# Kernel tuning notes

Hardware: AMD Instinct MI355X
Metric: run time of the kernel (lower is better)

The kernel has to match this reference:

```python
import jax, jax.numpy as jnp
import numpy as np

B, T, W, D = 4, 1000, 32, 200
ED, N, DCONV, DTR = 400, 16, 4, 13  # d_inner=2*d_model, d_state, d_conv, dt_rank=ceil(200/16)


def _causal_conv(x, w, b):
    # x: (B, L, ED), depthwise causal conv, kernel DCONV
    L = x.shape[1]
    xp = jnp.pad(x, ((0, 0), (DCONV - 1, 0), (0, 0)))
    y = sum(xp[:, k:k + L, :] * w[:, k] for k in range(DCONV))
    return y + b


def _ssm(x, A_log, Dp, xproj, dtw, dtb):
    # selective scan; x: (B, L, ED)
    A = -jnp.exp(A_log)                      # (ED, N)
    dbc = x @ xproj                          # (B, L, DTR+2N)
    delta, Bm, Cm = dbc[..., :DTR], dbc[..., DTR:DTR + N], dbc[..., DTR + N:]
    dt = jax.nn.softplus(delta @ dtw + dtb)  # (B, L, ED)
    dA = jnp.exp(dt[..., None] * A)                         # (B, L, ED, N)
    dBx = dt[..., None] * Bm[:, :, None, :] * x[..., None]  # (B, L, ED, N)

    def step(h, t):
        dA_t, dBx_t, C_t = t
        h = dA_t * h + dBx_t
        y = jnp.einsum('ben,bn->be', h, C_t)
        return h, y

    h0 = jnp.zeros((x.shape[0], ED, N), x.dtype)
    xs = (dA.transpose(1, 0, 2, 3), dBx.transpose(1, 0, 2, 3), Cm.transpose(1, 0, 2))
    _, ys = jax.lax.scan(step, h0, xs)
    return ys.transpose(1, 0, 2) + Dp * x


def _branch(x, in_proj, conv_w, conv_b, xproj, dtw, dtb, A_log, Dp):
    xz = x @ in_proj
    xp, z = xz[..., :ED], xz[..., ED:]
    xp = jax.nn.silu(_causal_conv(xp, conv_w, conv_b))
    y = _ssm(xp, A_log, Dp, xproj, dtw, dtb)
    return y * jax.nn.silu(z)


def setup_inputs() -> dict:
    key = jax.random.key(0)
    ks = jax.random.split(key, 24)
    s = 0.02
    nrm = lambda k, shape: jax.random.normal(k, shape, jnp.float32) * s
    inp = {}
    inp['input_ids'] = jax.random.normal(ks[0], (B, T, W, D), jnp.float32)
    inp['n_tweets'] = jax.random.randint(ks[1], (B,), 1, T + 1)
    inp['n_words'] = jax.random.randint(ks[2], (B, T), 1, W + 1)
    inp['cls_token'] = jnp.zeros((1, 1, D), jnp.float32)
    inp['w_attn'] = nrm(ks[3], (D, 1))
    inp['b_attn'] = jnp.zeros((1,), jnp.float32)
    inp['norm_w'] = jnp.ones((D,), jnp.float32)
    for i, d in enumerate(('f', 'b')):
        o = i * 8
        inp[f'in_proj_{d}'] = nrm(ks[4 + o], (D, 2 * ED))
        inp[f'conv_w_{d}'] = nrm(ks[5 + o], (ED, DCONV))
        inp[f'conv_b_{d}'] = jnp.zeros((ED,), jnp.float32)
        inp[f'xproj_{d}'] = nrm(ks[6 + o], (ED, DTR + 2 * N))
        inp[f'dtw_{d}'] = nrm(ks[7 + o], (DTR, ED))
        inp[f'dtb_{d}'] = jnp.zeros((ED,), jnp.float32)
        inp[f'A_log_{d}'] = jnp.log(jnp.broadcast_to(jnp.arange(1, N + 1, dtype=jnp.float32), (ED, N)))
        inp[f'D_{d}'] = jnp.ones((ED,), jnp.float32)
    inp['out_proj'] = nrm(ks[20], (ED, D))
    inp['head_w'] = nrm(ks[21], (D, 1))
    inp['head_b'] = jnp.zeros((1,), jnp.float32)
    return inp


def reference(input_ids, n_tweets, n_words, cls_token, w_attn, b_attn, norm_w,
              in_proj_f, conv_w_f, conv_b_f, xproj_f, dtw_f, dtb_f, A_log_f, D_f,
              in_proj_b, conv_w_b, conv_b_b, xproj_b, dtw_b, dtb_b, A_log_b, D_b,
              out_proj, head_w, head_b):
    Bz, Tz, Wz, Dz = input_ids.shape
    # ragged per-tweet attention pooling, fully vectorized with masks
    scores = jnp.squeeze(input_ids @ w_attn, -1) + b_attn[0]        # (B, T, W)
    wmask = jnp.arange(Wz) < n_words[..., None]                     # (B, T, W)
    scores = jnp.where(wmask, scores, -jnp.inf)
    attn = jax.nn.softmax(scores, axis=-1)
    tw = jnp.einsum('btw,btwd->btd', attn, input_ids)               # (B, T, D)
    tmask = jnp.arange(Tz) < n_tweets[:, None]
    tw = jnp.where(tmask[..., None], tw, 0.0)                       # padded tweets stay zero
    pos = Tz // 2
    x = jnp.concatenate([tw[:, :pos], jnp.broadcast_to(cls_token, (Bz, 1, Dz)), tw[:, pos:]], axis=1)
    # one bidirectional Mamba layer: pre-RMSNorm residual block
    xn = x * jax.lax.rsqrt(jnp.mean(x * x, axis=-1, keepdims=True) + 1e-5) * norm_w
    y_f = _branch(xn, in_proj_f, conv_w_f, conv_b_f, xproj_f, dtw_f, dtb_f, A_log_f, D_f)
    y_b = jnp.flip(_branch(jnp.flip(xn, 1), in_proj_b, conv_w_b, conv_b_b, xproj_b, dtw_b, dtb_b, A_log_b, D_b), 1)
    x = x + (y_f + y_b) @ out_proj
    logit = jnp.squeeze(x[:, pos] @ head_w, -1) + head_b[0]
    return jax.nn.sigmoid(logit)
```

## Files before the change

kernel.cpp:

```cpp
#include <hip/hip_runtime.h>
#include <cmath>

#define Bz 4
#define Tz 1000
#define Wz 32
#define Dz 200
#define EDz 400
#define Nz 16
#define DTRz 13
#define Lz 1001
#define POSz 500
#define LPz 501
#define TSTR 512
#define NEE 7
#define NEG_BIG -1e30f

__device__ __forceinline__ float wave_sum(float v) {
#pragma unroll
  for (int o = 32; o; o >>= 1) v += __shfl_xor(v, o);
  return v;
}

__global__ __launch_bounds__(256) void k_front(
    const float* __restrict__ x, const int* __restrict__ n_tweets,
    const int* __restrict__ n_words, const float* __restrict__ w_attn,
    const float* __restrict__ b_attn, const float* __restrict__ norm_w,
    const float* __restrict__ cls, const float* __restrict__ out_proj,
    const float* __restrict__ head_w, const float* __restrict__ ipf,
    const float* __restrict__ ipb, float* __restrict__ xn,
    float* __restrict__ zbuf, float* __restrict__ vbuf) {
  int bid = blockIdx.x;
  int tid = threadIdx.x;
  int wave = tid >> 6, lane = tid & 63;
  if (bid < 9) {
    if (bid == 0) {
      __shared__ float hw[Dz];
      if (tid < Dz) hw[tid] = head_w[tid];
      __syncthreads();
      for (int e = tid; e < EDz; e += 256) {
        float acc = 0.f;
        for (int d = 0; d < Dz; d += 4) {
          float4 ov = *(const float4*)(out_proj + e * Dz + d);
          acc += ov.x * hw[d] + ov.y * hw[d + 1] + ov.z * hw[d + 2] + ov.w * hw[d + 3];
        }
        vbuf[e] = acc;
      }
      return;
    }
    int id = bid - 1;
    int br = id >> 2, b = id & 3;
    __shared__ float xs[Dz];
    __shared__ float s_red[4];
    float val = (tid < Dz) ? cls[tid] : 0.f;
    float sq = wave_sum(val * val);
    if ((tid & 63) == 0) s_red[tid >> 6] = sq;
    __syncthreads();
    float tot = s_red[0] + s_red[1] + s_red[2] + s_red[3];
    float scale = rsqrtf(tot * (1.f / Dz) + 1e-5f);
    if (tid < Dz) {
      float o = val * scale * norm_w[tid];
      xs[tid] = o;
      if (br == 0) xn[((size_t)b * Lz + POSz) * Dz + tid] = o;
    }
    __syncthreads();
    const float* ip = br ? ipb : ipf;
    for (int e = tid; e < EDz; e += 256) {
      float acc = 0.f;
      for (int d = 0; d < Dz; ++d) acc += xs[d] * ip[d * (2 * EDz) + EDz + e];
      zbuf[((size_t)br * Bz + b) * EDz + e] = acc;
    }
    return;
  }
  int bt = (bid - 9) * 4 + wave;
  int b = bt / Tz, t = bt - b * Tz;
  int l = (t < POSz) ? t : t + 1;
  float* outr = xn + ((size_t)b * Lz + l) * Dz;
  int ntw = n_tweets[b]; if (ntw > Tz) ntw = Tz;
  if (t >= ntw) {
    if (lane < 50) *(float4*)(outr + lane * 4) = make_float4(0.f, 0.f, 0.f, 0.f);
    return;
  }
  int nw = n_words[b * Tz + t]; if (nw > Wz) nw = Wz; if (nw < 1) nw = 1;
  const float* xs = x + ((size_t)(b * Tz + t)) * (Wz * Dz);
  int h = lane & 1, w = lane >> 1;
  float sc = 0.f;
  if (w < nw) {
    const float* xr = xs + w * Dz + h * 100;
    const float* wr = w_attn + h * 100;
#pragma unroll
    for (int i = 0; i < 25; ++i) {
      float4 xv = *(const float4*)(xr + i * 4);
      float4 wv = *(const float4*)(wr + i * 4);
      sc += xv.x * wv.x + xv.y * wv.y + xv.z * wv.z + xv.w * wv.w;
    }
  }
  sc += __shfl_xor(sc, 1);
  float scv = (w < nw) ? (sc + b_attn[0]) : NEG_BIG;
  float m = scv;
#pragma unroll
  for (int o = 32; o; o >>= 1) m = fmaxf(m, __shfl_xor(m, o));
  float en = __expf(scv - m);
  float es = (h == 0) ? en : 0.f;
  float tot = wave_sum(es);
  en /= tot;
  float4 val = make_float4(0.f, 0.f, 0.f, 0.f);
  const float* xc = xs + lane * 4;
  for (int ww = 0; ww < nw; ++ww) {
    float aw = __shfl(en, 2 * ww);
    if (lane < 50) {
      float4 xv = *(const float4*)(xc + ww * Dz);
      val.x += aw * xv.x; val.y += aw * xv.y;
      val.z += aw * xv.z; val.w += aw * xv.w;
    }
  }
  float sq = (lane < 50) ? (val.x * val.x + val.y * val.y + val.z * val.z + val.w * val.w) : 0.f;
  sq = wave_sum(sq);
  float scale = rsqrtf(sq * (1.f / Dz) + 1e-5f);
  if (lane < 50) {
    float4 nw4 = *(const float4*)(norm_w + lane * 4);
    float4 o = make_float4(val.x * scale * nw4.x, val.y * scale * nw4.y,
                           val.z * scale * nw4.z, val.w * scale * nw4.w);
    *(float4*)(outr + lane * 4) = o;
  }
}

__global__ __launch_bounds__(256) void k_gemmid(
    const float* __restrict__ xn,
    const float* __restrict__ ipf, const float* __restrict__ ipb,
    const float* __restrict__ cwf, const float* __restrict__ cwb,
    const float* __restrict__ cbf, const float* __restrict__ cbb,
    const float* __restrict__ xpjf, const float* __restrict__ xpjb,
    float* __restrict__ xp_t, float* __restrict__ dbcp) {
  int bid = blockIdx.x;
  int ee = bid % NEE;
  int rem = bid / NEE;
  int tt = rem & 7, brb = rem >> 3;
  int br = brb >> 2, b = brb & 3;
  int t0 = tt * 64, e0 = ee * 64;
  int tid = threadIdx.x;
  int wave = tid >> 6, lane = tid & 63;
  const float* ip = br ? ipb : ipf;
  const float* cw = br ? cwb : cwf;
  const float* cb = br ? cbb : cbf;
  const float* xpj = br ? xpjb : xpjf;

  __shared__ float Xs[16][85];
  __shared__ float Ws[16][68];
  __shared__ float Pl[80][69];
  __shared__ float sred[4][64][45];

  int tx = tid & 15, ty = tid >> 4;
  float acc[5][4];
#pragma unroll
  for (int i = 0; i < 5; ++i)
#pragma unroll
    for (int j = 0; j < 4; ++j) acc[i][j] = 0.f;

  for (int dk = 0; dk < 200; dk += 16) {
    float xv[5];
#pragma unroll
    for (int r = 0; r < 5; ++r) {
      int trow = r * 16 + ty;
      int t = t0 - 8 + trow;
      int d = dk + tx;
      float v = 0.f;
      if (t >= 0 && t < LPz && d < Dz) {
        int l = br ? (Lz - 1 - t) : t;
        v = xn[((size_t)b * Lz + l) * Dz + d];
      }
      xv[r] = v;
    }
    int dw = dk + ty;
    int e4 = e0 + tx * 4;
    float wv[4];
#pragma unroll
    for (int c = 0; c < 4; ++c) {
      int e = e4 + c;
      wv[c] = (dw < Dz && e < EDz) ? ip[(size_t)dw * (2 * EDz) + e] : 0.f;
    }
    __syncthreads();
#pragma unroll
    for (int r = 0; r < 5; ++r) Xs[tx][r * 16 + ty] = xv[r];
#pragma unroll
    for (int c = 0; c < 4; ++c) Ws[ty][tx * 4 + c] = wv[c];
    __syncthreads();
#pragma unroll
    for (int k = 0; k < 16; ++k) {
      float av[5], bv[4];
#pragma unroll
      for (int i = 0; i < 5; ++i) av[i] = Xs[k][ty * 5 + i];
#pragma unroll
      for (int j = 0; j < 4; ++j) bv[j] = Ws[k][tx * 4 + j];
#pragma unroll
      for (int i = 0; i < 5; ++i)
#pragma unroll
        for (int j = 0; j < 4; ++j) acc[i][j] += av[i] * bv[j];
    }
  }
  __syncthreads();
#pragma unroll
  for (int i = 0; i < 5; ++i)
#pragma unroll
    for (int j = 0; j < 4; ++j) Pl[ty * 5 + i][tx * 4 + j] = acc[i][j];
  __syncthreads();

  float accq[45];
#pragma unroll
  for (int q = 0; q < 45; ++q) accq[q] = 0.f;
  int t = t0 + lane;
#pragma unroll 2
  for (int i = 0; i < 16; ++i) {
    int e_loc = wave * 16 + i;
    int e = e0 + e_loc;
    if (e < EDz) {
      int row = lane + 8;
      float p0 = Pl[row - 3][e_loc];
      float p1 = Pl[row - 2][e_loc];
      float p2 = Pl[row - 1][e_loc];
      float p3 = Pl[row][e_loc];
      float4 c4 = *(const float4*)(cw + e * 4);
      float a = cb[e] + c4.x * p0 + c4.y * p1 + c4.z * p2 + c4.w * p3;
      float sp = a / (1.f + __expf(-a));
      xp_t[((size_t)brb * EDz + e) * TSTR + t] = sp;
      const float* xq = xpj + e * 45;
#pragma unroll
      for (int q = 0; q < 45; ++q) accq[q] += sp * xq[q];
    }
  }
#pragma unroll
  for (int q = 0; q < 45; ++q) sred[wave][lane][q] = accq[q];
  __syncthreads();
  if (wave < 2) {
#pragma unroll
    for (int q = 0; q < 45; ++q)
      sred[wave][lane][q] += sred[wave + 2][lane][q];
  }
  __syncthreads();
  if (wave == 0) {
    float* dp = dbcp + ((size_t)(ee * 8 + brb) * 45) * TSTR + t;
#pragma unroll
    for (int q = 0; q < 45; ++q)
      dp[(size_t)q * TSTR] = sred[0][lane][q] + sred[1][lane][q];
  }
}

__global__ __launch_bounds__(256) void k_dt3(
    const float* __restrict__ dbcp, float* __restrict__ dfin_g,
    float* __restrict__ Bm_t, float* __restrict__ Cend) {
  int bid = blockIdx.x;
  int rg = bid & 3;
  int rem = bid >> 2;
  int tc = rem & 7, brb = rem >> 3;
  int tid = threadIdx.x;
  const size_t espstr = (size_t)8 * 45 * TSTR;
  int r0 = rg * 8;
  int nrows = (rg == 3) ? 5 : 8;
  for (int idx = tid; idx < nrows * 64; idx += 256) {
    int rl = idx >> 6, tl = idx & 63;
    int row = r0 + rl;
    size_t base = ((size_t)brb * 45 + row) * TSTR + tc * 64 + tl;
    float s = 0.f;
#pragma unroll
    for (int p = 0; p < NEE; ++p) s += dbcp[base + p * espstr];
    int tg = tc * 64 + tl;
    if (row < DTRz) dfin_g[((size_t)brb * DTRz + row) * TSTR + tg] = s;
    else Bm_t[((size_t)brb * Nz + (row - DTRz)) * TSTR + tg] = s;
  }
  if (rg == 3 && tc == 7 && tid < Nz) {
    size_t base = ((size_t)brb * 45 + 29 + tid) * TSTR + POSz;
    float s = 0.f;
#pragma unroll
    for (int p = 0; p < NEE; ++p) s += dbcp[base + p * espstr];
    Cend[brb * Nz + tid] = s;
  }
}

__global__ __launch_bounds__(64) void k_scan3(
    const float* __restrict__ xp_t, const float* __restrict__ dfin_g,
    const float* __restrict__ Bm_t, const float* __restrict__ Cend,
    const float* __restrict__ Alogf, const float* __restrict__ Alogb,
    const float* __restrict__ Dpf, const float* __restrict__ Dpb,
    const float* __restrict__ dtwf, const float* __restrict__ dtwb,
    const float* __restrict__ dtbf, const float* __restrict__ dtbb,
    const float* __restrict__ zbuf, const float* __restrict__ vbuf,
    float* __restrict__ ybuf) {
  int blk = blockIdx.x;
  int br = blk / (Bz * EDz);
  int rem = blk - br * (Bz * EDz);
  int b = rem / EDz, e = rem - b * EDz;
  int brb = br * Bz + b;
  int lane = threadIdx.x;
  const float* A_log = br ? Alogb : Alogf;
  const float* Dp = br ? Dpb : Dpf;
  const float* dtw = br ? dtwb : dtwf;
  const float* dtb = br ? dtbb : dtbf;
  float A[Nz];
  {
    const float4* ap = (const float4*)(A_log + e * Nz);
#pragma unroll
    for (int q = 0; q < 4; ++q) {
      float4 a4 = ap[q];
      A[q * 4 + 0] = -__expf(a4.x); A[q * 4 + 1] = -__expf(a4.y);
      A[q * 4 + 2] = -__expf(a4.z); A[q * 4 + 3] = -__expf(a4.w);
    }
  }
  float wq[DTRz];
#pragma unroll
  for (int q = 0; q < DTRz; ++q) wq[q] = dtw[q * EDz + e];
  float dtbe = dtb[e];
  const float* dfb = dfin_g + (size_t)brb * DTRz * TSTR;
  const float* xpp = xp_t + ((size_t)brb * EDz + e) * TSTR;
  const float* bmp = Bm_t + (size_t)brb * Nz * TSTR;

  float dtt_r[8];
  float loc = 0.f;
#pragma unroll
  for (int c = 0; c < 8; ++c) {
    int t = c * 64 + lane;
    float s = dtbe;
#pragma unroll
    for (int q = 0; q < DTRz; ++q) s += dfb[(size_t)q * TSTR + t] * wq[q];
    float dtv = (s > 20.f) ? s : log1pf(__expf(s));
    dtv = (t < LPz) ? dtv : 0.f;
    dtt_r[c] = dtv;
    loc += dtv;
  }
  float Stot = wave_sum(loc);
  float acc[Nz];
#pragma unroll
  for (int n = 0; n < Nz; ++n) acc[n] = 0.f;
  float carry = 0.f;
  for (int c = 0; c < 8; ++c) {
    int t = c * 64 + lane;
    bool act = t < LPz;
    float dtt = dtt_r[c];
    float xv = act ? xpp[t] : 0.f;
    float s = dtt;
#pragma unroll
    for (int o = 1; o < 64; o <<= 1) {
      float u = __shfl_up(s, o);
      s += (lane >= o) ? u : 0.f;
    }
    float S = carry + s;
    carry += __shfl(s, 63);
    float wt = dtt * xv;
    float decay = Stot - S;
#pragma unroll
    for (int n = 0; n < Nz; ++n) {
      float bv = act ? bmp[n * TSTR + t] : 0.f;
      acc[n] += __expf(A[n] * decay) * wt * bv;
    }
  }
#pragma unroll
  for (int o = 32; o; o >>= 1) {
#pragma unroll
    for (int n = 0; n < Nz; ++n) acc[n] += __shfl_xor(acc[n], o);
  }
  if (lane == 0) {
    float y = Dp[e] * xpp[LPz - 1];
#pragma unroll
    for (int n = 0; n < Nz; ++n) y += Cend[brb * Nz + n] * acc[n];
    float zz = zbuf[(size_t)brb * EDz + e];
    float sz = zz / (1.f + __expf(-zz));
    ybuf[(size_t)brb * EDz + e] = y * sz * vbuf[e];
  }
}

__global__ __launch_bounds__(256) void k_final(
    const float* __restrict__ cls, const float* __restrict__ head_w,
    const float* __restrict__ head_b, const float* __restrict__ ybuf,
    float* __restrict__ out) {
  int tid = threadIdx.x;
  int b = tid >> 6, lane = tid & 63;
  float acc = 0.f;
  for (int e = lane; e < EDz; e += 64)
    acc += ybuf[(size_t)b * EDz + e] + ybuf[(size_t)(Bz + b) * EDz + e];
  for (int d = lane; d < Dz; d += 64) acc += cls[d] * head_w[d];
  acc = wave_sum(acc);
  if (lane == 0) out[b] = 1.f / (1.f + __expf(-(acc + head_b[0])));
}

extern "C" void kernel_launch(void* const* d_in, const int* in_sizes, int n_in,
                              void* d_out, int out_size, void* d_ws, size_t ws_size,
                              hipStream_t stream) {
  const float* input_ids = (const float*)d_in[0];
  const int* n_tweets = (const int*)d_in[1];
  const int* n_words = (const int*)d_in[2];
  const float* cls = (const float*)d_in[3];
  const float* w_attn = (const float*)d_in[4];
  const float* b_attn = (const float*)d_in[5];
  const float* norm_w = (const float*)d_in[6];
  const float* ip[2] = {(const float*)d_in[7], (const float*)d_in[15]};
  const float* cw[2] = {(const float*)d_in[8], (const float*)d_in[16]};
  const float* cb[2] = {(const float*)d_in[9], (const float*)d_in[17]};
  const float* xpj[2] = {(const float*)d_in[10], (const float*)d_in[18]};
  const float* dtw[2] = {(const float*)d_in[11], (const float*)d_in[19]};
  const float* dtbp[2] = {(const float*)d_in[12], (const float*)d_in[20]};
  const float* Alog[2] = {(const float*)d_in[13], (const float*)d_in[21]};
  const float* Dpp[2] = {(const float*)d_in[14], (const float*)d_in[22]};
  const float* out_proj = (const float*)d_in[23];
  const float* head_w = (const float*)d_in[24];
  const float* head_b = (const float*)d_in[25];
  float* out = (float*)d_out;

  float* ws = (float*)d_ws;
  float* xn = ws;
  float* xp_t = xn + 800800;
  float* Bm_t = xp_t + 1638400;
  float* dbcp = Bm_t + 65536;
  float* dfin = dbcp + 1290240;
  float* Cend = dfin + 53248;
  float* zbuf = Cend + 128;
  float* vbuf = zbuf + 3200;
  float* ybuf = vbuf + 400;

  hipLaunchKernelGGL(k_front, dim3(9 + Bz * Tz / 4), dim3(256), 0, stream,
                     input_ids, n_tweets, n_words, w_attn, b_attn, norm_w,
                     cls, out_proj, head_w, ip[0], ip[1], xn, zbuf, vbuf);
  hipLaunchKernelGGL(k_gemmid, dim3(2 * Bz * 8 * NEE), dim3(256), 0, stream,
                     xn, ip[0], ip[1], cw[0], cw[1], cb[0], cb[1],
                     xpj[0], xpj[1], xp_t, dbcp);
  hipLaunchKernelGGL(k_dt3, dim3(2 * Bz * 8 * 4), dim3(256), 0, stream,
                     dbcp, dfin, Bm_t, Cend);
  hipLaunchKernelGGL(k_scan3, dim3(2 * Bz * EDz), dim3(64), 0, stream,
                     xp_t, dfin, Bm_t, Cend, Alog[0], Alog[1], Dpp[0], Dpp[1],
                     dtw[0], dtw[1], dtbp[0], dtbp[1], zbuf, vbuf, ybuf);
  hipLaunchKernelGGL(k_final, dim3(1), dim3(256), 0, stream,
                     cls, head_w, head_b, ybuf, out);
}
```

Before: 97.66 us.

## Replace partial-sum buffer and reduction kernel with atomic accumulation

The k_dt3 reduction kernel and the dbcp partial-sum buffer are removed. k_gemmid now atomically adds its per-e-chunk contributions straight into dfin, Bm_t and Cend, and extra k_front blocks zero those buffers first. This drops one kernel launch and a round trip of partial sums through global memory, at the cost of float atomics whose summation order varies between runs.

Result: no change. 95.86 us (-1.8%).

```diff
diff --git a/kernel.cpp b/kernel.cpp
--- a/kernel.cpp
+++ b/kernel.cpp
@@ -13,6 +13,8 @@
 #define LPz 501
 #define TSTR 512
 #define NEE 7
+#define NZB 8
+#define ZTOT 29728
 #define NEG_BIG -1e30f
 
 __device__ __forceinline__ float wave_sum(float v) {
@@ -28,7 +30,8 @@
     const float* __restrict__ cls, const float* __restrict__ out_proj,
     const float* __restrict__ head_w, const float* __restrict__ ipf,
     const float* __restrict__ ipb, float* __restrict__ xn,
-    float* __restrict__ zbuf, float* __restrict__ vbuf) {
+    float* __restrict__ zbuf, float* __restrict__ vbuf,
+    float* __restrict__ zero_base) {
   int bid = blockIdx.x;
   int tid = threadIdx.x;
   int wave = tid >> 6, lane = tid & 63;
@@ -71,7 +74,15 @@
     }
     return;
   }
-  int bt = (bid - 9) * 4 + wave;
+  if (bid < 9 + NZB) {
+    int zb = bid - 9;
+    float4* z = (float4*)zero_base;
+    int per = ZTOT / NZB;
+    for (int i = tid; i < per; i += 256)
+      z[zb * per + i] = make_float4(0.f, 0.f, 0.f, 0.f);
+    return;
+  }
+  int bt = (bid - 9 - NZB) * 4 + wave;
   int b = bt / Tz, t = bt - b * Tz;
   int l = (t < POSz) ? t : t + 1;
   float* outr = xn + ((size_t)b * Lz + l) * Dz;
@@ -130,7 +141,8 @@
     const float* __restrict__ cwf, const float* __restrict__ cwb,
     const float* __restrict__ cbf, const float* __restrict__ cbb,
     const float* __restrict__ xpjf, const float* __restrict__ xpjb,
-    float* __restrict__ xp_t, float* __restrict__ dbcp) {
+    float* __restrict__ xp_t, float* __restrict__ dfin_g,
+    float* __restrict__ Bm_t, float* __restrict__ Cend) {
   int bid = blockIdx.x;
   int ee = bid % NEE;
   int rem = bid / NEE;
@@ -237,41 +249,23 @@
   }
   __syncthreads();
   if (wave == 0) {
-    float* dp = dbcp + ((size_t)(ee * 8 + brb) * 45) * TSTR + t;
-#pragma unroll
-    for (int q = 0; q < 45; ++q)
-      dp[(size_t)q * TSTR] = sred[0][lane][q] + sred[1][lane][q];
-  }
-}
-
-__global__ __launch_bounds__(256) void k_dt3(
-    const float* __restrict__ dbcp, float* __restrict__ dfin_g,
-    float* __restrict__ Bm_t, float* __restrict__ Cend) {
-  int bid = blockIdx.x;
-  int rg = bid & 3;
-  int rem = bid >> 2;
-  int tc = rem & 7, brb = rem >> 3;
-  int tid = threadIdx.x;
-  const size_t espstr = (size_t)8 * 45 * TSTR;
-  int r0 = rg * 8;
-  int nrows = (rg == 3) ? 5 : 8;
-  for (int idx = tid; idx < nrows * 64; idx += 256) {
-    int rl = idx >> 6, tl = idx & 63;
-    int row = r0 + rl;
-    size_t base = ((size_t)brb * 45 + row) * TSTR + tc * 64 + tl;
-    float s = 0.f;
-#pragma unroll
-    for (int p = 0; p < NEE; ++p) s += dbcp[base + p * espstr];
-    int tg = tc * 64 + tl;
-    if (row < DTRz) dfin_g[((size_t)brb * DTRz + row) * TSTR + tg] = s;
-    else Bm_t[((size_t)brb * Nz + (row - DTRz)) * TSTR + tg] = s;
-  }
-  if (rg == 3 && tc == 7 && tid < Nz) {
-    size_t base = ((size_t)brb * 45 + 29 + tid) * TSTR + POSz;
-    float s = 0.f;
-#pragma unroll
-    for (int p = 0; p < NEE; ++p) s += dbcp[base + p * espstr];
-    Cend[brb * Nz + tid] = s;
+#pragma unroll
+    for (int q = 0; q < DTRz; ++q) {
+      float v = sred[0][lane][q] + sred[1][lane][q];
+      atomicAdd(&dfin_g[((size_t)brb * DTRz + q) * TSTR + t], v);
+    }
+#pragma unroll
+    for (int n = 0; n < Nz; ++n) {
+      float v = sred[0][lane][13 + n] + sred[1][lane][13 + n];
+      atomicAdd(&Bm_t[((size_t)brb * Nz + n) * TSTR + t], v);
+    }
+    if (tt == 7 && lane == (POSz - 448)) {
+#pragma unroll
+      for (int n = 0; n < Nz; ++n) {
+        float v = sred[0][lane][29 + n] + sred[1][lane][29 + n];
+        atomicAdd(&Cend[brb * Nz + n], v);
+      }
+    }
   }
 }
 
@@ -406,22 +400,19 @@
   float* ws = (float*)d_ws;
   float* xn = ws;
   float* xp_t = xn + 800800;
-  float* Bm_t = xp_t + 1638400;
-  float* dbcp = Bm_t + 65536;
-  float* dfin = dbcp + 1290240;
-  float* Cend = dfin + 53248;
+  float* dfin = xp_t + 1638400;
+  float* Bm_t = dfin + 53248;
+  float* Cend = Bm_t + 65536;
   float* zbuf = Cend + 128;
   float* vbuf = zbuf + 3200;
   float* ybuf = vbuf + 400;
 
-  hipLaunchKernelGGL(k_front, dim3(9 + Bz * Tz / 4), dim3(256), 0, stream,
+  hipLaunchKernelGGL(k_front, dim3(9 + NZB + Bz * Tz / 4), dim3(256), 0, stream,
                      input_ids, n_tweets, n_words, w_attn, b_attn, norm_w,
-                     cls, out_proj, head_w, ip[0], ip[1], xn, zbuf, vbuf);
+                     cls, out_proj, head_w, ip[0], ip[1], xn, zbuf, vbuf, dfin);
   hipLaunchKernelGGL(k_gemmid, dim3(2 * Bz * 8 * NEE), dim3(256), 0, stream,
                      xn, ip[0], ip[1], cw[0], cw[1], cb[0], cb[1],
-                     xpj[0], xpj[1], xp_t, dbcp);
-  hipLaunchKernelGGL(k_dt3, dim3(2 * Bz * 8 * 4), dim3(256), 0, stream,
-                     dbcp, dfin, Bm_t, Cend);
+                     xpj[0], xpj[1], xp_t, dfin, Bm_t, Cend);
   hipLaunchKernelGGL(k_scan3, dim3(2 * Bz * EDz), dim3(64), 0, stream,
                      xp_t, dfin, Bm_t, Cend, Alog[0], Alog[1], Dpp[0], Dpp[1],
                      dtw[0], dtw[1], dtbp[0], dtbp[1], zbuf, vbuf, ybuf);
```
